# Kernel tuning notes

Hardware: AMD Instinct MI355X
Metric: run time of the kernel (lower is better)

The kernel has to match this reference:

```python
import jax, jax.numpy as jnp
import numpy as np

B, L, D, N_HEADS = 8, 512, 1024, 16
D_HEAD = D // N_HEADS


def _mha_fuzzy(x_q, x_k, x_v, Wq, bq, Wk, bk, Wv, bv, Wo, bo):
    """Multi-head fuzzy attention, product t-norm score function."""
    b, lq, d_model = x_q.shape
    lk = x_k.shape[1]

    def proj(x, W, bias, l):
        # [b, l, D] -> [b, h, l, d_head]
        return (x @ W + bias).reshape(b, l, N_HEADS, D_HEAD).transpose(0, 2, 1, 3)

    Q = proj(x_q, Wq, bq, lq)
    K = proj(x_k, Wk, bk, lk)
    V = proj(x_v, Wv, bv, lk)
    # fuzzy memberships in [0,1]
    mu_q = jax.nn.sigmoid(Q)
    mu_k = jax.nn.sigmoid(K)
    # product t-norm aggregated over feature dim (mean), then softmax normalize
    scores = jnp.einsum('bhid,bhjd->bhij', mu_q, mu_k) / D_HEAD  # [b,h,lq,lk]
    attn = jax.nn.softmax(scores, axis=-1)
    out = jnp.einsum('bhij,bhjd->bhid', attn, V)
    out = out.transpose(0, 2, 1, 3).reshape(b, lq, d_model)
    return out @ Wo + bo, attn.mean(axis=1)  # avg over heads


def setup_inputs() -> dict:
    key = jax.random.key(0)
    ks = jax.random.split(key, 16)
    s = 1.0 / np.sqrt(D)
    inp = {
        'text_features': jax.random.normal(ks[0], (B, L, D), jnp.float32),
        'image_features': jax.random.normal(ks[1], (B, L, D), jnp.float32),
        'Wq': jax.random.normal(ks[2], (D, D), jnp.float32) * s,
        'bq': jnp.zeros((D,), jnp.float32),
        'Wk': jax.random.normal(ks[3], (D, D), jnp.float32) * s,
        'bk': jnp.zeros((D,), jnp.float32),
        'Wv': jax.random.normal(ks[4], (D, D), jnp.float32) * s,
        'bv': jnp.zeros((D,), jnp.float32),
        'Wo': jax.random.normal(ks[5], (D, D), jnp.float32) * s,
        'bo': jnp.zeros((D,), jnp.float32),
        'W1': jax.random.normal(ks[6], (3 * D, D), jnp.float32) * (1.0 / np.sqrt(3 * D)),
        'b1': jnp.zeros((D,), jnp.float32),
        'W2': jax.random.normal(ks[7], (D, D), jnp.float32) * s,
        'b2': jnp.zeros((D,), jnp.float32),
    }
    return inp


def reference(text_features, image_features, Wq, bq, Wk, bk, Wv, bv, Wo, bo, W1, b1, W2, b2):
    # shared fuzzy attention module applied in both cross-modal directions
    text_cross, avg_attn = _mha_fuzzy(text_features, image_features, image_features,
                                      Wq, bq, Wk, bk, Wv, bv, Wo, bo)
    image_cross, _ = _mha_fuzzy(image_features, text_features, text_features,
                                Wq, bq, Wk, bk, Wv, bv, Wo, bo)
    combined = jnp.concatenate([text_features, image_features, text_cross], axis=-1)
    hidden = jax.nn.relu(combined @ W1 + b1)
    compositional_output = hidden @ W2 + b2
    return text_cross, image_cross, compositional_output, avg_attn
```

## Files before the change

### kernel.cpp

```cpp
#include <hip/hip_runtime.h>

#define NB 8
#define SL 512
#define DM 1024
#define NH 16
#define DH 64

using bfrag = __attribute__((ext_vector_type(8))) short;
using facc  = __attribute__((ext_vector_type(4))) float;

__device__ __forceinline__ float bf2f(ushort u) {
    return __uint_as_float(((unsigned)u) << 16);
}
__device__ __forceinline__ ushort f2bf(float f) {
    unsigned x = __float_as_uint(f);
    return (ushort)((x + 0x7FFFu + ((x >> 16) & 1u)) >> 16);
}
__device__ __forceinline__ unsigned pack2(float a, float b) {
    return (unsigned)f2bf(a) | ((unsigned)f2bf(b) << 16);
}
__device__ __forceinline__ void gload16(const ushort* g, ushort* l) {
    __builtin_amdgcn_global_load_lds(
        (const __attribute__((address_space(1))) unsigned*)g,
        (__attribute__((address_space(3))) unsigned*)l, 16, 0, 0);
}

__device__ __forceinline__ void tconv_body(void* smem_,
                                           const float* __restrict__ W,
                                           ushort* __restrict__ WT,
                                           const int R, const int C,
                                           const int c0, const int r0) {
    ushort (*T)[68] = (ushort (*)[68])smem_;
    const int tid = threadIdx.x;
    #pragma unroll
    for (int rr = 0; rr < 4; ++rr) {
        const int r = (tid >> 4) + rr * 16;
        const int c4 = (tid & 15) * 4;
        const float4 f = *(const float4*)(W + (size_t)(r0 + r) * C + c0 + c4);
        T[c4+0][r] = f2bf(f.x); T[c4+1][r] = f2bf(f.y);
        T[c4+2][r] = f2bf(f.z); T[c4+3][r] = f2bf(f.w);
    }
    __syncthreads();
    #pragma unroll
    for (int rr = 0; rr < 4; ++rr) {
        const int c = (tid >> 4) + rr * 16;
        const int r4 = (tid & 15) * 4;
        *(ushort4*)(WT + (size_t)(c0 + c) * R + r0 + r4) =
            make_ushort4(T[c][r4+0], T[c][r4+1], T[c][r4+2], T[c][r4+3]);
    }
}

__global__ __launch_bounds__(256)
void prep_k(const float* __restrict__ text, const float* __restrict__ image,
            const float* __restrict__ Wq, const float* __restrict__ Wk,
            const float* __restrict__ Wv, const float* __restrict__ Wo,
            ushort* __restrict__ xbf, ushort* __restrict__ Wt,
            ushort* __restrict__ WoT)
{
    __shared__ ushort Tbuf[64][68];
    const int bid = blockIdx.x;
    const size_t SZc = (size_t)NB * SL * DM;
    if (bid < 8192) {
        const int half = bid >> 12;
        const float* s = half ? image : text;
        ushort* d = xbf + (size_t)half * SZc;
        const size_t i = ((size_t)(bid & 4095) * 256 + threadIdx.x) * 4;
        const float4 f = *(const float4*)(s + i);
        *(ushort4*)(d + i) =
            make_ushort4(f2bf(f.x), f2bf(f.y), f2bf(f.z), f2bf(f.w));
    } else {
        const int t = bid - 8192;
        const int wsel = t >> 8, tt = t & 255;
        const float* W = (wsel == 0) ? Wq : (wsel == 1) ? Wk
                       : (wsel == 2) ? Wv : Wo;
        ushort* WT = (wsel < 3) ? Wt + (size_t)wsel * DM * DM : WoT;
        tconv_body(Tbuf, W, WT, DM, DM, (tt & 15) * 64, (tt >> 4) * 64);
    }
}

__global__ __launch_bounds__(256)
void tconvW12_k(const float* __restrict__ W1, const float* __restrict__ W2,
                ushort* __restrict__ W1T, ushort* __restrict__ W2T)
{
    __shared__ ushort Tbuf[64][68];
    const int bid = blockIdx.x;
    if (bid < 768)
        tconv_body(Tbuf, W1, W1T, 3 * DM, DM, (bid & 15) * 64, (bid >> 4) * 64);
    else {
        const int t = bid - 768;
        tconv_body(Tbuf, W2, W2T, DM, DM, (t & 15) * 64, (t >> 4) * 64);
    }
}

template<int ACT, int OMODE>
__device__ __forceinline__ void gemm_body(
    void* smem_, const int L, const int NTg, const int MTg,
    const ushort* __restrict__ A0, const ushort* __restrict__ A1,
    const float* __restrict__ A2f, const ushort* __restrict__ A2b,
    const int KA1, const int KA2, const int Ktot,
    const int lda, const int ldaf,
    const ushort* __restrict__ AM1, const int Msplit,
    const ushort* __restrict__ BT, const int ldb,
    const float* __restrict__ bias, const float* __restrict__ biasK,
    const float* __restrict__ biasV,
    float* __restrict__ outf, ushort* __restrict__ outb,
    ushort* __restrict__ outbK, ushort* __restrict__ outbVT,
    const int clustN)
{
    ushort* sh = (ushort*)smem_;
    const int tid  = threadIdx.x;
    const int w    = tid >> 6;
    const int lane = tid & 63;
    const int ln   = lane & 15, qd = lane >> 4;
    const int wm = (w & 1) * 64, wn = (w >> 1) * 64;

    const int xcd = L & 7, sIdx = L >> 3;
    int mt, nt;
    if (clustN) { const int np = NTg >> 3; nt = xcd * np + sIdx % np; mt = sIdx / np; }
    else        { mt = xcd * (MTg >> 3) + sIdx / NTg; nt = sIdx - (sIdx / NTg) * NTg; }
    const int m0 = mt * 128, n0 = nt * 128;

    const ushort* A0u = A0; const ushort* A1u = A1; int m0A = m0;
    if (Msplit && m0 >= Msplit) { A0u = AM1; A1u = AM1; m0A = m0 - Msplit; }

    const int arow = (lane >> 3);
    const int kc8s = ((lane & 7) ^ arow) * 8;

    facc acc[4][4];
    #pragma unroll
    for (int i = 0; i < 4; ++i)
        #pragma unroll
        for (int j = 0; j < 4; ++j)
            acc[i][j] = (facc){0.f, 0.f, 0.f, 0.f};

    auto stage = [&](int k0, ushort* buf) {
        ushort* Asb = buf;
        ushort* Bsb = buf + 8192;
        #pragma unroll
        for (int t = 0; t < 4; ++t) {
            const int c = w * 4 + t;
            gload16(BT + (size_t)(n0 + c * 8 + arow) * ldb + k0 + kc8s,
                    &Bsb[c * 512]);
        }
        if (k0 < KA2) {
            const ushort* Ab; int ko;
            if (k0 < KA1) { Ab = A0u; ko = k0; }
            else          { Ab = A1u; ko = k0 - KA1; }
            #pragma unroll
            for (int t = 0; t < 4; ++t) {
                const int c = w * 4 + t;
                gload16(Ab + (size_t)(m0A + c * 8 + arow) * lda + ko + kc8s,
                        &Asb[c * 512]);
            }
        } else if (A2b) {
            const int ko = k0 - KA2;
            #pragma unroll
            for (int t = 0; t < 4; ++t) {
                const int c = w * 4 + t;
                gload16(A2b + (size_t)(m0A + c * 8 + arow) * ldaf + ko + kc8s,
                        &Asb[c * 512]);
            }
        } else {
            const int ko = k0 - KA2;
            #pragma unroll
            for (int t = 0; t < 4; ++t) {
                const int c = w * 4 + t;
                const float* src = A2f + (size_t)(m0A + c * 8 + arow) * ldaf + ko + kc8s;
                const float4 f0 = *(const float4*)src;
                const float4 f1 = *(const float4*)(src + 4);
                uint4 p;
                p.x = pack2(f0.x, f0.y); p.y = pack2(f0.z, f0.w);
                p.z = pack2(f1.x, f1.y); p.w = pack2(f1.z, f1.w);
                *(uint4*)&Asb[c * 512 + lane * 8] = p;
            }
        }
    };

    stage(0, sh);
    for (int k0 = 0; k0 < Ktot; k0 += 64) {
        ushort* cur = sh + ((k0 >> 6) & 1) * 16384;
        ushort* nxt = sh + (((k0 >> 6) & 1) ^ 1) * 16384;
        __syncthreads();
        if (k0 + 64 < Ktot) stage(k0 + 64, nxt);
        ushort* Asb = cur;
        ushort* Bsb = cur + 8192;
        #pragma unroll
        for (int ks = 0; ks < 2; ++ks) {
            const int ch = (ks * 4 + qd) ^ (ln & 7);
            bfrag af[4], bfv[4];
            #pragma unroll
            for (int i = 0; i < 4; ++i)
                af[i] = *(const bfrag*)&Asb[(wm + i*16 + ln) * 64 + ch * 8];
            #pragma unroll
            for (int j = 0; j < 4; ++j)
                bfv[j] = *(const bfrag*)&Bsb[(wn + j*16 + ln) * 64 + ch * 8];
            #pragma unroll
            for (int i = 0; i < 4; ++i)
                #pragma unroll
                for (int j = 0; j < 4; ++j)
                    acc[i][j] = __builtin_amdgcn_mfma_f32_16x16x32_bf16(
                        af[i], bfv[j], acc[i][j], 0, 0, 0);
        }
    }

    if (OMODE == 4) {
        const int seg   = n0 >> 10;
        const int nloc0 = n0 & 1023;
        const float* bs = (seg == 0) ? bias : (seg == 1) ? biasK : biasV;
        if (seg < 2) {
            ushort* ob = (seg == 0) ? outb : outbK;
            #pragma unroll
            for (int j = 0; j < 4; ++j) {
                const int nl = nloc0 + wn + j * 16 + ln;
                const float bn = bs[nl];
                #pragma unroll
                for (int i = 0; i < 4; ++i) {
                    const int mb = m0 + wm + i * 16 + qd * 4;
                    #pragma unroll
                    for (int r = 0; r < 4; ++r) {
                        const float v = 1.f / (1.f + __expf(-(acc[i][j][r] + bn)));
                        const int m = mb + r;
                        const int g = m >> 9, l = m & 511;
                        ob[(((size_t)(g * NH + (nl >> 6))) * SL + l) * DH + (nl & 63)]
                            = f2bf(v);
                    }
                }
            }
        } else {
            __syncthreads();
            #pragma unroll
            for (int j = 0; j < 4; ++j) {
                const int n_l = wn + j * 16 + ln;
                const float bn = bs[nloc0 + n_l];
                #pragma unroll
                for (int i = 0; i < 4; ++i) {
                    #pragma unroll
                    for (int r = 0; r < 4; ++r) {
                        const int m_l = wm + i * 16 + qd * 4 + r;
                        const int c = (m_l >> 3) ^ (n_l & 7);
                        sh[n_l * 128 + c * 8 + (m_l & 7)] = f2bf(acc[i][j][r] + bn);
                    }
                }
            }
            __syncthreads();
            const int n_l = tid >> 1, half = tid & 1;
            const int nl = nloc0 + n_l;
            const int g = m0 >> 9, l0 = m0 & 511;
            ushort* dst = outbVT +
                (((size_t)(g * NH + (nl >> 6))) * DH + (nl & 63)) * SL + l0;
            #pragma unroll
            for (int u = 0; u < 8; ++u) {
                const int c = half * 8 + u;
                const int cs = c ^ (n_l & 7);
                *(uint4*)(dst + c * 8) = *(const uint4*)&sh[n_l * 128 + cs * 8];
            }
        }
        return;
    }

    #pragma unroll
    for (int j = 0; j < 4; ++j) {
        const int n = n0 + wn + j * 16 + ln;
        const float bn = bias[n];
        #pragma unroll
        for (int i = 0; i < 4; ++i) {
            const int mb = m0 + wm + i * 16 + qd * 4;
            #pragma unroll
            for (int r = 0; r < 4; ++r) {
                float v = acc[i][j][r] + bn;
                if (ACT == 1)      v = 1.f / (1.f + __expf(-v));
                else if (ACT == 2) v = v > 0.f ? v : 0.f;
                const int m = mb + r;
                if (OMODE == 0)      outf[(size_t)m * DM + n] = v;
                else if (OMODE == 2) outb[(size_t)m * DM + n] = f2bf(v);
                else {
                    outf[(size_t)m * DM + n] = v;
                    if (m < Msplit) outb[(size_t)m * DM + n] = f2bf(v);
                }
            }
        }
    }
}

template<int ACT, int OMODE>
__global__ __launch_bounds__(256, 2)
void mfma_gemm(const ushort* __restrict__ A0, const ushort* __restrict__ A1,
               const float* __restrict__ A2f, const ushort* __restrict__ A2b,
               const int KA1, const int KA2, const int Ktot,
               const int lda, const int ldaf,
               const ushort* __restrict__ AM1, const int Msplit,
               const ushort* __restrict__ BT, const int ldb,
               const float* __restrict__ bias, const float* __restrict__ biasK,
               const float* __restrict__ biasV,
               float* __restrict__ outf, ushort* __restrict__ outb,
               ushort* __restrict__ outbK, ushort* __restrict__ outbVT,
               const int clustN)
{
    __shared__ char smem[65536];
    gemm_body<ACT, OMODE>(smem, blockIdx.x + gridDim.x * blockIdx.y,
                          gridDim.x, gridDim.y,
                          A0, A1, A2f, A2b, KA1, KA2, Ktot, lda, ldaf,
                          AM1, Msplit, BT, ldb, bias, biasK, biasV,
                          outf, outb, outbK, outbVT, clustN);
}

__global__ __launch_bounds__(256, 2)
void attn2m_k(const ushort* __restrict__ Qm, const ushort* __restrict__ Km,
              const ushort* __restrict__ VTm, ushort* __restrict__ AO0,
              ushort* __restrict__ AO1, float* __restrict__ RS0,
              float* __restrict__ RS1)
{
    __shared__ ushort Ks[128 * 64];
    __shared__ ushort VTs[64 * 128];
    __shared__ ushort Es[128 * 128];
    const int tid  = threadIdx.x;
    const int w    = tid >> 6;
    const int lane = tid & 63;
    const int ln   = lane & 15, qd = lane >> 4;
    const int wm  = (w & 1) * 64;
    const int wns = (w >> 1) * 64;
    const int wnd = (w >> 1) * 32;

    const int L   = blockIdx.x;
    const int xcd = L & 7, s = L >> 3;
    const int qt  = s & 3;
    const int pid = xcd * 32 + (s >> 2);
    const int h   = pid & 15;
    const int zz  = pid >> 4;
    const int dir = zz >> 3, b = zz & 7;

    const size_t HALFc = (size_t)NB * SL * DM;
    const ushort* Qall = Qm  + (dir ? HALFc : 0);
    const ushort* Kall = Km  + (dir ? 0 : HALFc);
    const ushort* Vall = VTm + (dir ? 0 : HALFc);
    ushort* AOp = dir ? AO1 : AO0;
    float*  RSp = dir ? RS1 : RS0;

    const size_t ho = ((size_t)(b * NH + h)) * SL * DH;
    const ushort* Qg  = Qall + ho + (size_t)qt * 128 * DH;
    const ushort* Kg  = Kall + ho;
    const ushort* VTg = Vall + ho;

    bfrag qf[4][2];
    #pragma unroll
    for (int i = 0; i < 4; ++i)
        #pragma unroll
        for (int ks = 0; ks < 2; ++ks)
            qf[i][ks] = *(const bfrag*)(Qg + (size_t)(wm + i*16 + ln) * DH + ks*32 + qd*8);

    facc oacc[4][2];
    #pragma unroll
    for (int i = 0; i < 4; ++i)
        #pragma unroll
        for (int j = 0; j < 2; ++j)
            oacc[i][j] = (facc){0.f, 0.f, 0.f, 0.f};
    float rp[4];
    #pragma unroll
    for (int i = 0; i < 4; ++i)
        rp[i] = 0.f;

    const int arow = lane >> 3;
    const int kc8s = ((lane & 7) ^ arow) * 8;
    const int vrow = lane >> 4;

    for (int kc = 0; kc < 4; ++kc) {
        __syncthreads();
        #pragma unroll
        for (int t = 0; t < 4; ++t) {
            const int c = w * 4 + t;
            const int vc8s = ((lane & 15) ^ ((c * 4 + vrow) & 7)) * 8;
            gload16(Kg + (size_t)(kc*128 + c*8 + arow) * DH + kc8s, &Ks[c * 512]);
            gload16(VTg + (size_t)(c*4 + vrow) * SL + kc*128 + vc8s, &VTs[c * 512]);
        }
        __syncthreads();

        facc sacc[4][4];
        #pragma unroll
        for (int j = 0; j < 4; ++j)
            #pragma unroll
            for (int i = 0; i < 4; ++i)
                sacc[j][i] = (facc){0.f, 0.f, 0.f, 0.f};
        #pragma unroll
        for (int ks = 0; ks < 2; ++ks) {
            const int ch = (ks * 4 + qd) ^ (ln & 7);
            bfrag kf[4];
            #pragma unroll
            for (int j = 0; j < 4; ++j)
                kf[j] = *(const bfrag*)&Ks[(wns + j*16 + ln) * 64 + ch * 8];
            #pragma unroll
            for (int j = 0; j < 4; ++j)
                #pragma unroll
                for (int i = 0; i < 4; ++i)
                    sacc[j][i] = __builtin_amdgcn_mfma_f32_16x16x32_bf16(
                        kf[j], qf[i][ks], sacc[j][i], 0, 0, 0);
        }

        #pragma unroll
        for (int i = 0; i < 4; ++i) {
            const int q  = wm + i*16 + ln;
            const int qs = q & 7;
            float p = 0.f;
            #pragma unroll
            for (int j = 0; j < 4; ++j) {
                const int key0 = wns + j*16 + qd*4;
                const float e0 = __expf(sacc[j][i][0] * 0.015625f);
                const float e1 = __expf(sacc[j][i][1] * 0.015625f);
                const float e2 = __expf(sacc[j][i][2] * 0.015625f);
                const float e3 = __expf(sacc[j][i][3] * 0.015625f);
                const int c = ((key0 & 127) >> 3) ^ qs;
                uint2 pk;
                pk.x = pack2(e0, e1);
                pk.y = pack2(e2, e3);
                *(uint2*)&Es[q * 128 + c * 8 + (key0 & 7)] = pk;
                p += (e0 + e1) + (e2 + e3);
            }
            rp[i] += p;
        }
        __syncthreads();

        #pragma unroll
        for (int ks2 = 0; ks2 < 4; ++ks2) {
            const int vch = (ks2 * 4 + qd) ^ (ln & 7);
            bfrag ea[4], vb[2];
            #pragma unroll
            for (int i = 0; i < 4; ++i) {
                const int q = wm + i*16 + ln;
                const int cs = (ks2*4 + qd) ^ (q & 7);
                ea[i] = *(const bfrag*)&Es[q * 128 + cs * 8];
            }
            #pragma unroll
            for (int j = 0; j < 2; ++j)
                vb[j] = *(const bfrag*)&VTs[(wnd + j*16 + ln) * 128 + vch * 8];
            #pragma unroll
            for (int i = 0; i < 4; ++i)
                #pragma unroll
                for (int j = 0; j < 2; ++j)
                    oacc[i][j] = __builtin_amdgcn_mfma_f32_16x16x32_bf16(
                        ea[i], vb[j], oacc[i][j], 0, 0, 0);
        }
    }

    #pragma unroll
    for (int i = 0; i < 4; ++i) {
        float p = rp[i];
        p += __shfl_xor(p, 16);
        p += __shfl_xor(p, 32);
        rp[i] = p;
    }

    __syncthreads();
    float* rsls = (float*)Ks;
    if (qd == 0) {
        #pragma unroll
        for (int i = 0; i < 4; ++i)
            rsls[(w >> 1) * 128 + wm + i*16 + ln] = rp[i];
    }
    __syncthreads();
    if (tid < 128) {
        const float t = rsls[tid] + rsls[128 + tid];
        RSp[(size_t)(b * NH + h) * SL + qt * 128 + tid] = t;
        rsls[tid] = t;
    }
    __syncthreads();

    #pragma unroll
    for (int i = 0; i < 4; ++i) {
        #pragma unroll
        for (int r = 0; r < 4; ++r) {
            const int q = wm + i*16 + qd*4 + r;
            const float inv = 1.f / rsls[q];
            const size_t rowo = ((size_t)(b*SL + qt*128 + q)) * DM + h*DH;
            #pragma unroll
            for (int j = 0; j < 2; ++j)
                AOp[rowo + wnd + j*16 + ln] = f2bf(oacc[i][j][r] * inv);
        }
    }
}

__device__ __forceinline__ void avg3_body(void* smem_, const int kt,
                                          const int qt, const int b,
                                          const ushort* __restrict__ Qm,
                                          const ushort* __restrict__ Km,
                                          const float* __restrict__ RS,
                                          float* __restrict__ avga)
{
    ushort* Qs = (ushort*)smem_;
    ushort* Kt = Qs + 64 * 64;
    float* rss = (float*)(Kt + 64 * 64);
    const int tid  = threadIdx.x;
    const int w    = tid >> 6;
    const int lane = tid & 63;
    const int ln   = lane & 15, qd = lane >> 4;
    const int wq = (w & 1) * 32, wk = (w >> 1) * 32;

    const int arow = lane >> 3;
    const int kc8s = ((lane & 7) ^ arow) * 8;

    float acc[2][2][4];
    #pragma unroll
    for (int i = 0; i < 2; ++i)
        #pragma unroll
        for (int j = 0; j < 2; ++j)
            #pragma unroll
            for (int r = 0; r < 4; ++r)
                acc[i][j][r] = 0.f;

    for (int h = 0; h < NH; ++h) {
        const size_t ho = ((size_t)(b * NH + h)) * SL * DH;
        __syncthreads();
        #pragma unroll
        for (int t = 0; t < 2; ++t) {
            const int c = w * 2 + t;
            gload16(Qm + ho + (size_t)(qt*64 + c*8 + arow) * DH + kc8s, &Qs[c * 512]);
            gload16(Km + ho + (size_t)(kt*64 + c*8 + arow) * DH + kc8s, &Kt[c * 512]);
        }
        if (tid < 64) rss[tid] = RS[(size_t)(b*NH + h)*SL + qt*64 + tid];
        __syncthreads();

        facc s[2][2];
        #pragma unroll
        for (int i = 0; i < 2; ++i)
            #pragma unroll
            for (int j = 0; j < 2; ++j)
                s[i][j] = (facc){0.f, 0.f, 0.f, 0.f};
        #pragma unroll
        for (int ks = 0; ks < 2; ++ks) {
            const int ch = (ks * 4 + qd) ^ (ln & 7);
            bfrag qa[2], kb[2];
            #pragma unroll
            for (int i = 0; i < 2; ++i)
                qa[i] = *(const bfrag*)&Qs[(wq + i*16 + ln) * 64 + ch * 8];
            #pragma unroll
            for (int j = 0; j < 2; ++j)
                kb[j] = *(const bfrag*)&Kt[(wk + j*16 + ln) * 64 + ch * 8];
            #pragma unroll
            for (int i = 0; i < 2; ++i)
                #pragma unroll
                for (int j = 0; j < 2; ++j)
                    s[i][j] = __builtin_amdgcn_mfma_f32_16x16x32_bf16(
                        qa[i], kb[j], s[i][j], 0, 0, 0);
        }
        #pragma unroll
        for (int i = 0; i < 2; ++i) {
            #pragma unroll
            for (int r = 0; r < 4; ++r) {
                const float ir = 0.0625f / rss[wq + i*16 + qd*4 + r];
                #pragma unroll
                for (int j = 0; j < 2; ++j)
                    acc[i][j][r] += __expf(s[i][j][r] * 0.015625f) * ir;
            }
        }
    }
    #pragma unroll
    for (int i = 0; i < 2; ++i) {
        #pragma unroll
        for (int r = 0; r < 4; ++r) {
            const int q = wq + i*16 + qd*4 + r;
            #pragma unroll
            for (int j = 0; j < 2; ++j)
                avga[((size_t)(b*SL + qt*64 + q)) * SL + kt*64 + wk + j*16 + ln]
                    = acc[i][j][r];
        }
    }
}

__global__ __launch_bounds__(256, 2)
void mid_k(const ushort* __restrict__ AOt, const ushort* __restrict__ AOi,
           const ushort* __restrict__ WoT, const float* __restrict__ bo,
           float* __restrict__ text_cross, ushort* __restrict__ tcb,
           const ushort* __restrict__ Qm, const ushort* __restrict__ Km,
           const float* __restrict__ RS, float* __restrict__ avga,
           const float* __restrict__ W1, const float* __restrict__ W2,
           ushort* __restrict__ W1T, ushort* __restrict__ W2T)
{
    __shared__ char smem[65536];
    const int bid = blockIdx.x;
    if (bid < 1024) {
        if (bid & 1) {
            const int la = bid >> 1;
            avg3_body(smem, la & 7, (la >> 3) & 7, la >> 6, Qm, Km, RS, avga);
        } else {
            gemm_body<0, 5>(smem, bid >> 1, 8, 64,
                AOt, AOt, nullptr, nullptr, DM, DM, DM, DM, DM,
                AOi, 4096, WoT, DM, bo, nullptr, nullptr,
                text_cross, tcb, nullptr, nullptr, 0);
        }
    } else {
        const int t = bid - 1024;
        if (t < 768)
            tconv_body(smem, W1, W1T, 3 * DM, DM, (t & 15) * 64, (t >> 4) * 64);
        else {
            const int u = t - 768;
            tconv_body(smem, W2, W2T, DM, DM, (u & 15) * 64, (u >> 4) * 64);
        }
    }
}

extern "C" void kernel_launch(void* const* d_in, const int* in_sizes, int n_in,
                              void* d_out, int out_size, void* d_ws, size_t ws_size,
                              hipStream_t stream)
{
    (void)in_sizes; (void)n_in; (void)out_size;
    const float* text  = (const float*)d_in[0];
    const float* image = (const float*)d_in[1];
    const float* Wq = (const float*)d_in[2];
    const float* bq = (const float*)d_in[3];
    const float* Wk = (const float*)d_in[4];
    const float* bk = (const float*)d_in[5];
    const float* Wv = (const float*)d_in[6];
    const float* bv = (const float*)d_in[7];
    const float* Wo = (const float*)d_in[8];
    const float* bo = (const float*)d_in[9];
    const float* W1 = (const float*)d_in[10];
    const float* b1 = (const float*)d_in[11];
    const float* W2 = (const float*)d_in[12];
    const float* b2 = (const float*)d_in[13];
    float* out = (float*)d_out;

    const size_t SZ   = (size_t)NB * SL * DM;
    const size_t HALF = SZ;

    ushort* xbf = (ushort*)d_ws;
    ushort* Qb  = xbf + 2*SZ;
    ushort* Kb  = Qb  + 2*SZ;
    ushort* VT  = Kb  + 2*SZ;
    ushort* AOt = VT  + 2*SZ;
    ushort* Wt  = AOt + SZ;
    float*  RS  = (float*)(Wt + 3*DM*DM);
    char*   wsEnd = (char*)(RS + NB*NH*SL);
    ushort* hidden = Qb;

    float* text_cross = out;
    float* comp       = out + 2*SZ;
    float* avga       = out + 3*SZ;

    const size_t extBytes = (size_t)NB*NH*SL*4 + (size_t)DM*DM*2
                          + (size_t)SZ*2 + (size_t)DM*DM*2;
    const size_t fixBytes = (size_t)(wsEnd - (char*)d_ws);
    float* RS2; ushort* WoT; ushort* AOi; ushort* W2T;
    const bool ext = (ws_size >= fixBytes + extBytes);
    if (ext) {
        RS2 = (float*)wsEnd;
        WoT = (ushort*)(RS2 + NB*NH*SL);
        AOi = WoT + DM*DM;
        W2T = AOi + SZ;
    } else {
        WoT = (ushort*)comp;
        AOi = WoT + DM*DM;
        RS2 = (float*)Wt;
        W2T = AOt;
    }

    const dim3 blk(256);

    prep_k<<<9216, blk, 0, stream>>>(text, image, Wq, Wk, Wv, Wo, xbf, Wt, WoT);

    mfma_gemm<0,4><<<dim3(24,64), blk, 0, stream>>>(
        xbf, xbf, nullptr, nullptr, DM, DM, DM, DM, DM, nullptr, 0,
        Wt, DM, bq, bk, bv, nullptr, Qb, Kb, VT, 1);

    attn2m_k<<<dim3(1024), blk, 0, stream>>>(Qb, Kb, VT, AOt, AOi, RS, RS2);

    if (ext) {
        mid_k<<<2048, blk, 0, stream>>>(AOt, AOi, WoT, bo, text_cross, Kb,
                                        Qb, Kb + HALF, RS, avga, W1, W2, Wt, W2T);
    } else {
        mid_k<<<1024, blk, 0, stream>>>(AOt, AOi, WoT, bo, text_cross, Kb,
                                        Qb, Kb + HALF, RS, avga, W1, W2, Wt, W2T);
        tconvW12_k<<<1024, blk, 0, stream>>>(W1, W2, Wt, W2T);
    }

    mfma_gemm<2,2><<<dim3(8,32), blk, 0, stream>>>(
        xbf, xbf + SZ, nullptr, Kb, DM, 2*DM, 3*DM, DM, DM, nullptr, 0,
        Wt, 3*DM, b1, nullptr, nullptr, nullptr, hidden, nullptr, nullptr, 0);
    mfma_gemm<0,0><<<dim3(8,32), blk, 0, stream>>>(
        hidden, hidden, nullptr, nullptr, DM, DM, DM, DM, DM, nullptr, 0,
        W2T, DM, b2, nullptr, nullptr, comp, nullptr, nullptr, nullptr, 0);
}
```

Before: 332.2 us.

## Move W1/W2 transposes into prep kernel and run FFN GEMMs with 8 waves

```diff
diff --git a/kernel.cpp b/kernel.cpp
--- a/kernel.cpp
+++ b/kernel.cpp
@@ -54,8 +54,10 @@
 void prep_k(const float* __restrict__ text, const float* __restrict__ image,
             const float* __restrict__ Wq, const float* __restrict__ Wk,
             const float* __restrict__ Wv, const float* __restrict__ Wo,
+            const float* __restrict__ W1, const float* __restrict__ W2,
             ushort* __restrict__ xbf, ushort* __restrict__ Wt,
-            ushort* __restrict__ WoT)
+            ushort* __restrict__ WoT, ushort* __restrict__ W1T,
+            ushort* __restrict__ W2T)
 {
     __shared__ ushort Tbuf[64][68];
     const int bid = blockIdx.x;
@@ -68,13 +70,21 @@
         const float4 f = *(const float4*)(s + i);
         *(ushort4*)(d + i) =
             make_ushort4(f2bf(f.x), f2bf(f.y), f2bf(f.z), f2bf(f.w));
-    } else {
+    } else if (bid < 9216) {
         const int t = bid - 8192;
         const int wsel = t >> 8, tt = t & 255;
         const float* W = (wsel == 0) ? Wq : (wsel == 1) ? Wk
                        : (wsel == 2) ? Wv : Wo;
         ushort* WT = (wsel < 3) ? Wt + (size_t)wsel * DM * DM : WoT;
         tconv_body(Tbuf, W, WT, DM, DM, (tt & 15) * 64, (tt >> 4) * 64);
+    } else {
+        const int t = bid - 9216;
+        if (t < 768)
+            tconv_body(Tbuf, W1, W1T, 3 * DM, DM, (t & 15) * 64, (t >> 4) * 64);
+        else {
+            const int u = t - 768;
+            tconv_body(Tbuf, W2, W2T, DM, DM, (u & 15) * 64, (u >> 4) * 64);
+        }
     }
 }
 
@@ -92,7 +102,7 @@
     }
 }
 
-template<int ACT, int OMODE>
+template<int ACT, int OMODE, int WAVES>
 __device__ __forceinline__ void gemm_body(
     void* smem_, const int L, const int NTg, const int MTg,
     const ushort* __restrict__ A0, const ushort* __restrict__ A1,
@@ -107,12 +117,15 @@
     ushort* __restrict__ outbK, ushort* __restrict__ outbVT,
     const int clustN)
 {
+    constexpr int NJ = (WAVES == 4) ? 4 : 2;
+    constexpr int TC = 16 / WAVES;
     ushort* sh = (ushort*)smem_;
     const int tid  = threadIdx.x;
     const int w    = tid >> 6;
     const int lane = tid & 63;
     const int ln   = lane & 15, qd = lane >> 4;
-    const int wm = (w & 1) * 64, wn = (w >> 1) * 64;
+    const int wm = (w & 1) * 64;
+    const int wn = (WAVES == 4) ? (w >> 1) * 64 : (w >> 1) * 32;
 
     const int xcd = L & 7, sIdx = L >> 3;
     int mt, nt;
@@ -126,19 +139,19 @@
     const int arow = (lane >> 3);
     const int kc8s = ((lane & 7) ^ arow) * 8;
 
-    facc acc[4][4];
+    facc acc[4][NJ];
     #pragma unroll
     for (int i = 0; i < 4; ++i)
         #pragma unroll
-        for (int j = 0; j < 4; ++j)
+        for (int j = 0; j < NJ; ++j)
             acc[i][j] = (facc){0.f, 0.f, 0.f, 0.f};
 
     auto stage = [&](int k0, ushort* buf) {
         ushort* Asb = buf;
         ushort* Bsb = buf + 8192;
         #pragma unroll
-        for (int t = 0; t < 4; ++t) {
-            const int c = w * 4 + t;
+        for (int t = 0; t < TC; ++t) {
+            const int c = w * TC + t;
             gload16(BT + (size_t)(n0 + c * 8 + arow) * ldb + k0 + kc8s,
                     &Bsb[c * 512]);
         }
@@ -147,24 +160,24 @@
             if (k0 < KA1) { Ab = A0u; ko = k0; }
             else          { Ab = A1u; ko = k0 - KA1; }
             #pragma unroll
-            for (int t = 0; t < 4; ++t) {
-                const int c = w * 4 + t;
+            for (int t = 0; t < TC; ++t) {
+                const int c = w * TC + t;
                 gload16(Ab + (size_t)(m0A + c * 8 + arow) * lda + ko + kc8s,
                         &Asb[c * 512]);
             }
         } else if (A2b) {
             const int ko = k0 - KA2;
             #pragma unroll
-            for (int t = 0; t < 4; ++t) {
-                const int c = w * 4 + t;
+            for (int t = 0; t < TC; ++t) {
+                const int c = w * TC + t;
                 gload16(A2b + (size_t)(m0A + c * 8 + arow) * ldaf + ko + kc8s,
                         &Asb[c * 512]);
             }
         } else {
             const int ko = k0 - KA2;
             #pragma unroll
-            for (int t = 0; t < 4; ++t) {
-                const int c = w * 4 + t;
+            for (int t = 0; t < TC; ++t) {
+                const int c = w * TC + t;
                 const float* src = A2f + (size_t)(m0A + c * 8 + arow) * ldaf + ko + kc8s;
                 const float4 f0 = *(const float4*)src;
                 const float4 f1 = *(const float4*)(src + 4);
@@ -187,30 +200,30 @@
         #pragma unroll
         for (int ks = 0; ks < 2; ++ks) {
             const int ch = (ks * 4 + qd) ^ (ln & 7);
-            bfrag af[4], bfv[4];
+            bfrag af[4], bfv[NJ];
             #pragma unroll
             for (int i = 0; i < 4; ++i)
                 af[i] = *(const bfrag*)&Asb[(wm + i*16 + ln) * 64 + ch * 8];
             #pragma unroll
-            for (int j = 0; j < 4; ++j)
+            for (int j = 0; j < NJ; ++j)
                 bfv[j] = *(const bfrag*)&Bsb[(wn + j*16 + ln) * 64 + ch * 8];
             #pragma unroll
             for (int i = 0; i < 4; ++i)
                 #pragma unroll
-                for (int j = 0; j < 4; ++j)
+                for (int j = 0; j < NJ; ++j)
                     acc[i][j] = __builtin_amdgcn_mfma_f32_16x16x32_bf16(
                         af[i], bfv[j], acc[i][j], 0, 0, 0);
         }
     }
 
-    if (OMODE == 4) {
+    if constexpr (OMODE == 4) {
         const int seg   = n0 >> 10;
         const int nloc0 = n0 & 1023;
         const float* bs = (seg == 0) ? bias : (seg == 1) ? biasK : biasV;
         if (seg < 2) {
             ushort* ob = (seg == 0) ? outb : outbK;
             #pragma unroll
-            for (int j = 0; j < 4; ++j) {
+            for (int j = 0; j < NJ; ++j) {
                 const int nl = nloc0 + wn + j * 16 + ln;
                 const float bn = bs[nl];
                 #pragma unroll
@@ -229,7 +242,7 @@
         } else {
             __syncthreads();
             #pragma unroll
-            for (int j = 0; j < 4; ++j) {
+            for (int j = 0; j < NJ; ++j) {
                 const int n_l = wn + j * 16 + ln;
                 const float bn = bs[nloc0 + n_l];
                 #pragma unroll
@@ -256,34 +269,34 @@
             }
         }
         return;
-    }
-
-    #pragma unroll
-    for (int j = 0; j < 4; ++j) {
-        const int n = n0 + wn + j * 16 + ln;
-        const float bn = bias[n];
-        #pragma unroll
-        for (int i = 0; i < 4; ++i) {
-            const int mb = m0 + wm + i * 16 + qd * 4;
-            #pragma unroll
-            for (int r = 0; r < 4; ++r) {
-                float v = acc[i][j][r] + bn;
-                if (ACT == 1)      v = 1.f / (1.f + __expf(-v));
-                else if (ACT == 2) v = v > 0.f ? v : 0.f;
-                const int m = mb + r;
-                if (OMODE == 0)      outf[(size_t)m * DM + n] = v;
-                else if (OMODE == 2) outb[(size_t)m * DM + n] = f2bf(v);
-                else {
-                    outf[(size_t)m * DM + n] = v;
-                    if (m < Msplit) outb[(size_t)m * DM + n] = f2bf(v);
+    } else {
+        #pragma unroll
+        for (int j = 0; j < NJ; ++j) {
+            const int n = n0 + wn + j * 16 + ln;
+            const float bn = bias[n];
+            #pragma unroll
+            for (int i = 0; i < 4; ++i) {
+                const int mb = m0 + wm + i * 16 + qd * 4;
+                #pragma unroll
+                for (int r = 0; r < 4; ++r) {
+                    float v = acc[i][j][r] + bn;
+                    if (ACT == 1)      v = 1.f / (1.f + __expf(-v));
+                    else if (ACT == 2) v = v > 0.f ? v : 0.f;
+                    const int m = mb + r;
+                    if (OMODE == 0)      outf[(size_t)m * DM + n] = v;
+                    else if (OMODE == 2) outb[(size_t)m * DM + n] = f2bf(v);
+                    else {
+                        outf[(size_t)m * DM + n] = v;
+                        if (m < Msplit) outb[(size_t)m * DM + n] = f2bf(v);
+                    }
                 }
             }
         }
     }
 }
 
-template<int ACT, int OMODE>
-__global__ __launch_bounds__(256, 2)
+template<int ACT, int OMODE, int WAVES>
+__global__ __launch_bounds__(WAVES * 64, 2)
 void mfma_gemm(const ushort* __restrict__ A0, const ushort* __restrict__ A1,
                const float* __restrict__ A2f, const ushort* __restrict__ A2b,
                const int KA1, const int KA2, const int Ktot,
@@ -297,11 +310,11 @@
                const int clustN)
 {
     __shared__ char smem[65536];
-    gemm_body<ACT, OMODE>(smem, blockIdx.x + gridDim.x * blockIdx.y,
-                          gridDim.x, gridDim.y,
-                          A0, A1, A2f, A2b, KA1, KA2, Ktot, lda, ldaf,
-                          AM1, Msplit, BT, ldb, bias, biasK, biasV,
-                          outf, outb, outbK, outbVT, clustN);
+    gemm_body<ACT, OMODE, WAVES>(smem, blockIdx.x + gridDim.x * blockIdx.y,
+                                 gridDim.x, gridDim.y,
+                                 A0, A1, A2f, A2b, KA1, KA2, Ktot, lda, ldaf,
+                                 AM1, Msplit, BT, ldb, bias, biasK, biasV,
+                                 outf, outb, outbK, outbVT, clustN);
 }
 
 __global__ __launch_bounds__(256, 2)
@@ -569,30 +582,18 @@
            const ushort* __restrict__ WoT, const float* __restrict__ bo,
            float* __restrict__ text_cross, ushort* __restrict__ tcb,
            const ushort* __restrict__ Qm, const ushort* __restrict__ Km,
-           const float* __restrict__ RS, float* __restrict__ avga,
-           const float* __restrict__ W1, const float* __restrict__ W2,
-           ushort* __restrict__ W1T, ushort* __restrict__ W2T)
+           const float* __restrict__ RS, float* __restrict__ avga)
 {
     __shared__ char smem[65536];
     const int bid = blockIdx.x;
-    if (bid < 1024) {
-        if (bid & 1) {
-            const int la = bid >> 1;
-            avg3_body(smem, la & 7, (la >> 3) & 7, la >> 6, Qm, Km, RS, avga);
-        } else {
-            gemm_body<0, 5>(smem, bid >> 1, 8, 64,
-                AOt, AOt, nullptr, nullptr, DM, DM, DM, DM, DM,
-                AOi, 4096, WoT, DM, bo, nullptr, nullptr,
-                text_cross, tcb, nullptr, nullptr, 0);
-        }
+    if (bid & 1) {
+        const int la = bid >> 1;
+        avg3_body(smem, la & 7, (la >> 3) & 7, la >> 6, Qm, Km, RS, avga);
     } else {
-        const int t = bid - 1024;
-        if (t < 768)
-            tconv_body(smem, W1, W1T, 3 * DM, DM, (t & 15) * 64, (t >> 4) * 64);
-        else {
-            const int u = t - 768;
-            tconv_body(smem, W2, W2T, DM, DM, (u & 15) * 64, (u >> 4) * 64);
-        }
+        gemm_body<0, 5, 4>(smem, bid >> 1, 8, 64,
+            AOt, AOt, nullptr, nullptr, DM, DM, DM, DM, DM,
+            AOi, 4096, WoT, DM, bo, nullptr, nullptr,
+            text_cross, tcb, nullptr, nullptr, 0);
     }
 }
 
@@ -634,46 +635,47 @@
     float* comp       = out + 2*SZ;
     float* avga       = out + 3*SZ;
 
-    const size_t extBytes = (size_t)NB*NH*SL*4 + (size_t)DM*DM*2
-                          + (size_t)SZ*2 + (size_t)DM*DM*2;
+    const size_t extA = (size_t)NB*NH*SL*4 + (size_t)DM*DM*2
+                      + (size_t)SZ*2 + (size_t)DM*DM*2;
+    const size_t extB = extA + (size_t)3*DM*DM*2;
     const size_t fixBytes = (size_t)(wsEnd - (char*)d_ws);
-    float* RS2; ushort* WoT; ushort* AOi; ushort* W2T;
-    const bool ext = (ws_size >= fixBytes + extBytes);
-    if (ext) {
+    float* RS2; ushort* WoT; ushort* AOi; ushort* W2T; ushort* W1Tx;
+    const bool haveA = (ws_size >= fixBytes + extA);
+    const bool haveB = (ws_size >= fixBytes + extB);
+    if (haveA) {
         RS2 = (float*)wsEnd;
         WoT = (ushort*)(RS2 + NB*NH*SL);
         AOi = WoT + DM*DM;
         W2T = AOi + SZ;
+        W1Tx = haveB ? (W2T + DM*DM) : Wt;
     } else {
         WoT = (ushort*)comp;
         AOi = WoT + DM*DM;
         RS2 = (float*)Wt;
         W2T = AOt;
+        W1Tx = Wt;
     }
 
     const dim3 blk(256);
 
-    prep_k<<<9216, blk, 0, stream>>>(text, image, Wq, Wk, Wv, Wo, xbf, Wt, WoT);
-
-    mfma_gemm<0,4><<<dim3(24,64), blk, 0, stream>>>(
+    prep_k<<<haveB ? 10240 : 9216, blk, 0, stream>>>(
+        text, image, Wq, Wk, Wv, Wo, W1, W2, xbf, Wt, WoT, W1Tx, W2T);
+
+    mfma_gemm<0,4,4><<<dim3(24,64), blk, 0, stream>>>(
         xbf, xbf, nullptr, nullptr, DM, DM, DM, DM, DM, nullptr, 0,
         Wt, DM, bq, bk, bv, nullptr, Qb, Kb, VT, 1);
 
     attn2m_k<<<dim3(1024), blk, 0, stream>>>(Qb, Kb, VT, AOt, AOi, RS, RS2);
 
-    if (ext) {
-        mid_k<<<2048, blk, 0, stream>>>(AOt, AOi, WoT, bo, text_cross, Kb,
-                                        Qb, Kb + HALF, RS, avga, W1, W2, Wt, W2T);
-    } else {
-        mid_k<<<1024, blk, 0, stream>>>(AOt, AOi, WoT, bo, text_cross, Kb,
-                                        Qb, Kb + HALF, RS, avga, W1, W2, Wt, W2T);
-        tconvW12_k<<<1024, blk, 0, stream>>>(W1, W2, Wt, W2T);
-    }
-
-    mfma_gemm<2,2><<<dim3(8,32), blk, 0, stream>>>(
+    mid_k<<<1024, blk, 0, stream>>>(AOt, AOi, WoT, bo, text_cross, Kb,
+                                    Qb, Kb + HALF, RS, avga);
+    if (!haveB)
+        tconvW12_k<<<1024, blk, 0, stream>>>(W1, W2, W1Tx, W2T);
+
+    mfma_gemm<2,2,8><<<dim3(8,32), dim3(512), 0, stream>>>(
         xbf, xbf + SZ, nullptr, Kb, DM, 2*DM, 3*DM, DM, DM, nullptr, 0,
-        Wt, 3*DM, b1, nullptr, nullptr, nullptr, hidden, nullptr, nullptr, 0);
-    mfma_gemm<0,0><<<dim3(8,32), blk, 0, stream>>>(
+        W1Tx, 3*DM, b1, nullptr, nullptr, nullptr, hidden, nullptr, nullptr, 0);
+    mfma_gemm<0,0,8><<<dim3(8,32), dim3(512), 0, stream>>>(
         hidden, hidden, nullptr, nullptr, DM, DM, DM, DM, DM, nullptr, 0,
         W2T, DM, b2, nullptr, nullptr, comp, nullptr, nullptr, nullptr, 0);
 }
```

After: 322.8 us (median of 2 runs). -2.8%, faster.
